# Kernel tuning notes

Hardware: AMD Instinct MI355X
Metric: run time of the kernel (lower is better)

## Reference

```python
import jax, jax.numpy as jnp
import numpy as np

CHANNELS = 32
HIDDEN = 1024
LAYERS = 8
NODE_TYPES = 7
N_NODES = 500_000
N_EDGES = 2_000_000
NUM_GRAPHS = 1024


def setup_inputs() -> dict:
    key = jax.random.key(0)
    ks = jax.random.split(key, 8)
    nodes = jax.random.randint(ks[0], (N_NODES,), 0, NODE_TYPES)
    sources = jax.random.randint(ks[1], (N_EDGES,), 0, N_NODES)
    targets = jax.random.randint(ks[2], (N_EDGES,), 0, N_NODES)
    # sorted graph ids covering all NUM_GRAPHS graphs (no empty graphs)
    batch = (jnp.arange(N_NODES) * NUM_GRAPHS) // N_NODES
    emb = jax.random.normal(ks[3], (NODE_TYPES, CHANNELS), dtype=jnp.float32)
    # xavier-normal-ish init for the 8 layers x {out, back} 32x32 convs
    xavier_std = (2.0 / (CHANNELS + CHANNELS)) ** 0.5
    conv_w = jax.random.normal(ks[4], (LAYERS, 2, CHANNELS, CHANNELS), dtype=jnp.float32) * xavier_std
    hidden_w = jax.random.normal(ks[5], (CHANNELS, HIDDEN), dtype=jnp.float32) * 0.05
    hidden_b = jax.random.normal(ks[6], (HIDDEN,), dtype=jnp.float32) * 0.05
    out_w = jax.random.normal(ks[7], (HIDDEN, 1), dtype=jnp.float32) * 0.05
    return dict(nodes=nodes, sources=sources, targets=targets, batch=batch,
                emb=emb, conv_w=conv_w, hidden_w=hidden_w, hidden_b=hidden_b,
                out_w=out_w)


def reference(nodes, sources, targets, batch, emb, conv_w, hidden_w, hidden_b, out_w):
    n = nodes.shape[0]
    ones_e = jnp.ones(sources.shape[0], dtype=jnp.float32)
    # norm = 1 / (1 + in-degree), norm_t = 1 / (1 + out-degree)  [N,1]
    norm = (1.0 / (1.0 + jax.ops.segment_sum(ones_e, targets, num_segments=n)))[:, None]
    norm_t = (1.0 / (1.0 + jax.ops.segment_sum(ones_e, sources, num_segments=n)))[:, None]
    node_counts = jax.ops.segment_sum(jnp.ones(n, dtype=jnp.float32), batch,
                                      num_segments=NUM_GRAPHS)

    x = emb[nodes]  # [N, C]

    def conv(x, s, t, nrm, w):
        # x.index_add(0, t, x[s]) -> x + scatter_add of gathered source feats
        agg = nrm * (x + jax.ops.segment_sum(x[s], t, num_segments=n))
        return jax.nn.relu(agg @ w)

    for l in range(LAYERS):
        x = x + conv(x, sources, targets, norm, conv_w[l, 0]) \
              + conv(x, targets, sources, norm_t, conv_w[l, 1])

    # mean pooling per graph
    g = jax.ops.segment_sum(x, batch, num_segments=NUM_GRAPHS) / node_counts[:, None]
    h = jax.nn.relu(g @ hidden_w + hidden_b)
    return (h @ out_w).squeeze(-1)  # [NUM_GRAPHS]
```

## Files before the change

### kernel.cpp

```cpp
#include <hip/hip_runtime.h>

#define CHANNELS 32
#define HIDDEN 1024
#define LAYERS 8
#define NRANGE 8

typedef __attribute__((ext_vector_type(8))) short short8;
typedef __attribute__((ext_vector_type(4))) float float4v;

__device__ __forceinline__ short f2bf_rne(float f) {
    union { float f; unsigned u; } v; v.f = f;
    unsigned r = v.u + 0x7fffu + ((v.u >> 16) & 1u);
    return (short)(r >> 16);
}
__device__ __forceinline__ float bfu2f(unsigned short h) {
    union { float f; unsigned u; } v; v.u = ((unsigned)h) << 16;
    return v.f;
}


__global__ __launch_bounds__(256)
void deg_range_kernel(const int* __restrict__ src, const int* __restrict__ tgt,
                      int* __restrict__ deg2, int n_nodes, int n_edges, int rsh) {
    int r = blockIdx.x & (NRANGE - 1);
    int chunk = blockIdx.x >> 3;
    int base = chunk * 2048;
#pragma unroll
    for (int j = 0; j < 8; j++) {
        int e = base + j * 256 + threadIdx.x;
        if (e < n_edges) {
            int t = __builtin_nontemporal_load(tgt + e);
            int s = __builtin_nontemporal_load(src + e);
            if ((t >> rsh) == r) atomicAdd(&deg2[t], 1);
            if ((s >> rsh) == r) atomicAdd(&deg2[n_nodes + s], 1);
        }
    }
}


__global__ __launch_bounds__(256)
void scan_pass1(const int* __restrict__ deg, int* __restrict__ bs, int n) {
    __shared__ int sh[256];
    int t = threadIdx.x;
    int base = blockIdx.x * 2048 + t * 8;
    int s = 0;
#pragma unroll
    for (int j = 0; j < 8; j++) { int idx = base + j; if (idx < n) s += deg[idx]; }
    sh[t] = s; __syncthreads();
    for (int st = 128; st > 0; st >>= 1) { if (t < st) sh[t] += sh[t + st]; __syncthreads(); }
    if (t == 0) bs[blockIdx.x] = sh[0];
}

__global__ void scan_pass2(int* __restrict__ bs, int nb) {
    __shared__ int sh[1024];
    int t = threadIdx.x;
    int v = (t < nb) ? bs[t] : 0;
    sh[t] = v; __syncthreads();
    for (int off = 1; off < 1024; off <<= 1) {
        int u = (t >= off) ? sh[t - off] : 0; __syncthreads();
        sh[t] += u; __syncthreads();
    }
    if (t < nb) bs[t] = sh[t] - v;
}

__global__ __launch_bounds__(256)
void scan_pass3(const int* __restrict__ deg, const int* __restrict__ bs,
                int* __restrict__ off, int n) {
    __shared__ int sh[256];
    int t = threadIdx.x;
    int base = blockIdx.x * 2048 + t * 8;
    int v[8]; int s = 0;
#pragma unroll
    for (int j = 0; j < 8; j++) { int idx = base + j; v[j] = (idx < n) ? deg[idx] : 0; s += v[j]; }
    sh[t] = s; __syncthreads();
    for (int st = 1; st < 256; st <<= 1) {
        int u = (t >= st) ? sh[t - st] : 0; __syncthreads();
        sh[t] += u; __syncthreads();
    }
    int acc = bs[blockIdx.x] + sh[t] - s;
#pragma unroll
    for (int j = 0; j < 8; j++) { int idx = base + j; if (idx < n) off[idx] = acc; acc += v[j]; }
}


__global__ __launch_bounds__(256)
void scatter_range_kernel(const int* __restrict__ src, const int* __restrict__ tgt,
                          int* __restrict__ cur2, int* __restrict__ nbr,
                          int n_nodes, int n_edges, int rsh, int rbase) {
    int r = rbase + (blockIdx.x & (NRANGE - 1));
    int chunk = blockIdx.x >> 3;
    int base = chunk * 2048;
#pragma unroll
    for (int j = 0; j < 8; j++) {
        int e = base + j * 256 + threadIdx.x;
        if (e < n_edges) {
            int t = __builtin_nontemporal_load(tgt + e);
            int s = __builtin_nontemporal_load(src + e);
            if ((t >> rsh) == r) { int p = atomicAdd(&cur2[t], 1);           nbr[p] = s; }
            if ((s >> rsh) == r) { int q = atomicAdd(&cur2[n_nodes + s], 1); nbr[q] = t; }
        }
    }
}


__global__ __launch_bounds__(256)
void init_kernel(const int* __restrict__ nodes, const float* __restrict__ emb,
                 const int* __restrict__ deg2,
                 float* __restrict__ x, unsigned short* __restrict__ xg,
                 float* __restrict__ norm, float* __restrict__ norm_t, int n_nodes) {
    int gid = blockIdx.x * blockDim.x + threadIdx.x;
    int i = gid >> 5, c = gid & 31;
    if (i >= n_nodes) return;
    float v = emb[nodes[i] * CHANNELS + c];
    x[gid] = v;
    xg[gid] = (unsigned short)f2bf_rne(v);
    if (c == 0) {
        norm[i]   = 1.0f / (1.0f + (float)deg2[i]);
        norm_t[i] = 1.0f / (1.0f + (float)deg2[n_nodes + i]);
    }
}


__global__ void counts_kernel(const int* __restrict__ batch, float* __restrict__ counts,
                              int n_nodes, int n_graphs) {
    int b = blockIdx.x * blockDim.x + threadIdx.x;
    if (b >= n_graphs) return;
    int lo = 0, hi = n_nodes;
    while (lo < hi) { int mid = (lo + hi) >> 1; if (batch[mid] < b) lo = mid + 1; else hi = mid; }
    int s = lo;
    lo = 0; hi = n_nodes;
    while (lo < hi) { int mid = (lo + hi) >> 1; if (batch[mid] < b + 1) lo = mid + 1; else hi = mid; }
    counts[b] = (float)(lo - s);
}


__global__ __launch_bounds__(256, 8)
void layer_mfma(const int* __restrict__ off2, const int* __restrict__ nbr,
                const float* __restrict__ wbase,
                const float* __restrict__ norm, const float* __restrict__ norm_t,
                float* __restrict__ x,
                const unsigned short* __restrict__ xgin,
                unsigned short* __restrict__ xgout,
                int n_nodes, int n_edges) {
    __shared__ short A1h[64][32], A2h[64][32];
    __shared__ short W0h[32][32], W1h[32][32];
    __shared__ int offIn[65], offOut[65];

    int tid = threadIdx.x;
    int nodeblock = blockIdx.x * 64;

    for (int idx = tid; idx < CHANNELS * CHANNELS; idx += 256) {
        int k = idx >> 5, n = idx & 31;
        W0h[n][k] = f2bf_rne(wbase[idx]);
        W1h[n][k] = f2bf_rne(wbase[CHANNELS * CHANNELS + idx]);
    }
    if (tid < 65) {
        int idx = nodeblock + tid;
        offIn[tid]  = (idx <= n_nodes) ? off2[idx] : n_edges;
        int idx2 = n_nodes + idx;
        offOut[tid] = (idx2 < 2 * n_nodes) ? off2[idx2] : 2 * n_edges;
    }
    __syncthreads();

    int c = tid & 31, g = tid >> 5;

    int bi_c, d1_c, bo_c, d2_c, nbl1_c, nbl2_c, node_c;
    float xv_c;
    {
        int local = g;
        node_c = nodeblock + local;
        bi_c = offIn[local];  d1_c = offIn[local + 1] - bi_c;
        bo_c = offOut[local]; d2_c = offOut[local + 1] - bo_c;
        nbl1_c = (c < d1_c) ? nbr[bi_c + c] : 0;
        nbl2_c = (c < d2_c) ? nbr[bo_c + c] : 0;
        xv_c = (node_c < n_nodes) ? x[node_c * CHANNELS + c] : 0.f;
    }

    for (int pass = 0; pass < 8; pass++) {
        int bi_n = 0, d1_n = 0, bo_n = 0, d2_n = 0, nbl1_n = 0, nbl2_n = 0, node_n = 0;
        float xv_n = 0.f;
        if (pass < 7) {
            int local = (pass + 1) * 8 + g;
            node_n = nodeblock + local;
            bi_n = offIn[local];  d1_n = offIn[local + 1] - bi_n;
            bo_n = offOut[local]; d2_n = offOut[local + 1] - bo_n;
            nbl1_n = (c < d1_n) ? nbr[bi_n + c] : 0;
            nbl2_n = (c < d2_n) ? nbr[bo_n + c] : 0;
            xv_n = (node_n < n_nodes) ? x[node_n * CHANNELS + c] : 0.f;
        }

        int local = pass * 8 + g;
        int i = node_c;
        int self = (i < n_nodes) ? i : 0;

        int m1 = d1_c < 32 ? d1_c : 32;
        int m2 = d2_c < 32 ? d2_c : 32;
        int mm = m1 > m2 ? m1 : m2;

        float a1 = 0.f, a2 = 0.f;
        for (int j = 0; j < mm; j += 4) {
            int p0 = __shfl(nbl1_c, (j)     & 31, 32);
            int p1 = __shfl(nbl1_c, (j + 1) & 31, 32);
            int p2 = __shfl(nbl1_c, (j + 2) & 31, 32);
            int p3 = __shfl(nbl1_c, (j + 3) & 31, 32);
            int q0 = __shfl(nbl2_c, (j)     & 31, 32);
            int q1 = __shfl(nbl2_c, (j + 1) & 31, 32);
            int q2 = __shfl(nbl2_c, (j + 2) & 31, 32);
            int q3 = __shfl(nbl2_c, (j + 3) & 31, 32);
            p0 = (j     < m1) ? p0 : self;
            p1 = (j + 1 < m1) ? p1 : self;
            p2 = (j + 2 < m1) ? p2 : self;
            p3 = (j + 3 < m1) ? p3 : self;
            q0 = (j     < m2) ? q0 : self;
            q1 = (j + 1 < m2) ? q1 : self;
            q2 = (j + 2 < m2) ? q2 : self;
            q3 = (j + 3 < m2) ? q3 : self;
            float u0 = bfu2f(xgin[p0 * CHANNELS + c]);
            float u1 = bfu2f(xgin[p1 * CHANNELS + c]);
            float u2 = bfu2f(xgin[p2 * CHANNELS + c]);
            float u3 = bfu2f(xgin[p3 * CHANNELS + c]);
            float w0 = bfu2f(xgin[q0 * CHANNELS + c]);
            float w1 = bfu2f(xgin[q1 * CHANNELS + c]);
            float w2 = bfu2f(xgin[q2 * CHANNELS + c]);
            float w3 = bfu2f(xgin[q3 * CHANNELS + c]);
            a1 += (j     < m1) ? u0 : 0.f;
            a1 += (j + 1 < m1) ? u1 : 0.f;
            a1 += (j + 2 < m1) ? u2 : 0.f;
            a1 += (j + 3 < m1) ? u3 : 0.f;
            a2 += (j     < m2) ? w0 : 0.f;
            a2 += (j + 1 < m2) ? w1 : 0.f;
            a2 += (j + 2 < m2) ? w2 : 0.f;
            a2 += (j + 3 < m2) ? w3 : 0.f;
        }
        for (int e = bi_c + 32; e < bi_c + d1_c; e++) a1 += bfu2f(xgin[nbr[e] * CHANNELS + c]);
        for (int e = bo_c + 32; e < bo_c + d2_c; e++) a2 += bfu2f(xgin[nbr[e] * CHANNELS + c]);

        if (i < n_nodes) {
            float n1 = norm[i], n2 = norm_t[i];
            a1 = n1 * (xv_c + a1);
            a2 = n2 * (xv_c + a2);
            A1h[local][c] = f2bf_rne(a1);
            A2h[local][c] = f2bf_rne(a2);
        } else {
            A1h[local][c] = 0;
            A2h[local][c] = 0;
        }

        bi_c = bi_n; d1_c = d1_n; bo_c = bo_n; d2_c = d2_n;
        nbl1_c = nbl1_n; nbl2_c = nbl2_n; xv_c = xv_n; node_c = node_n;
    }
    __syncthreads();

    int wv = tid >> 6, lane = tid & 63;
    int m = lane & 15, quad = lane >> 4;
    int row0 = wv * 16;

    short8 a1h = *(const short8*)&A1h[row0 + m][quad * 8];
    short8 a2h = *(const short8*)&A2h[row0 + m][quad * 8];

    float4v dd[4];
#pragma unroll
    for (int h = 0; h < 2; h++) {
        int n0 = h * 16 + m;
        short8 b0h = *(const short8*)&W0h[n0][quad * 8];
        short8 b1h = *(const short8*)&W1h[n0][quad * 8];
        float4v d1 = {0.f, 0.f, 0.f, 0.f};
        d1 = __builtin_amdgcn_mfma_f32_16x16x32_bf16(a1h, b0h, d1, 0, 0, 0);
        float4v d2 = {0.f, 0.f, 0.f, 0.f};
        d2 = __builtin_amdgcn_mfma_f32_16x16x32_bf16(a2h, b1h, d2, 0, 0, 0);
        dd[h * 2] = d1; dd[h * 2 + 1] = d2;
    }

#pragma unroll
    for (int h = 0; h < 2; h++) {
        float4v d1 = dd[h * 2], d2 = dd[h * 2 + 1];
#pragma unroll
        for (int r = 0; r < 4; r++) {
            int local = row0 + quad * 4 + r;
            int node = nodeblock + local;
            if (node < n_nodes) {
                int col = h * 16 + m;
                float v = x[node * CHANNELS + col] + fmaxf(d1[r], 0.f) + fmaxf(d2[r], 0.f);
                x[node * CHANNELS + col] = v;
                xgout[node * CHANNELS + col] = (unsigned short)f2bf_rne(v);
            }
        }
    }
}


#define POOL_CHUNK 2048

__global__ __launch_bounds__(256)
void pool_kernel(const int* __restrict__ batch, const float* __restrict__ x,
                 float* __restrict__ g, int n_nodes) {
    int c = threadIdx.x & 31;
    int r = threadIdx.x >> 5;
    int base = blockIdx.x * POOL_CHUNK;
    float acc = 0.f;
    int cur = -1;
    for (int it = 0; it < POOL_CHUNK / 8; it++) {
        int node = base + it * 8 + r;
        if (node >= n_nodes) break;
        int b = batch[node];
        if (b != cur) {
            if (cur >= 0) atomicAdd(&g[cur * CHANNELS + c], acc);
            acc = 0.f;
            cur = b;
        }
        acc += x[node * CHANNELS + c];
    }
    if (cur >= 0) atomicAdd(&g[cur * CHANNELS + c], acc);
}


__global__ __launch_bounds__(256)
void mlp_kernel(const float* __restrict__ g, const float* __restrict__ counts,
                const float* __restrict__ hidden_w, const float* __restrict__ hidden_b,
                const float* __restrict__ out_w, float* __restrict__ out) {
    __shared__ float grow[CHANNELS];
    __shared__ float red[256];
    int graph = blockIdx.x;
    int tid = threadIdx.x;
    if (tid < CHANNELS) grow[tid] = g[graph * CHANNELS + tid] / counts[graph];
    __syncthreads();
    float partial = 0.f;
    for (int q = 0; q < HIDDEN / 256; q++) {
        int j = q * 256 + tid;
        float h = hidden_b[j];
#pragma unroll
        for (int k = 0; k < CHANNELS; k++) h += grow[k] * hidden_w[k * HIDDEN + j];
        partial += fmaxf(h, 0.f) * out_w[j];
    }
    red[tid] = partial;
    __syncthreads();
    for (int s = 128; s > 0; s >>= 1) {
        if (tid < s) red[tid] += red[tid + s];
        __syncthreads();
    }
    if (tid == 0) out[graph] = red[0];
}


extern "C" void kernel_launch(void* const* d_in, const int* in_sizes, int n_in,
                              void* d_out, int out_size, void* d_ws, size_t ws_size,
                              hipStream_t stream) {
    const int*   nodes    = (const int*)d_in[0];
    const int*   sources  = (const int*)d_in[1];
    const int*   targets  = (const int*)d_in[2];
    const int*   batch    = (const int*)d_in[3];
    const float* emb      = (const float*)d_in[4];
    const float* conv_w   = (const float*)d_in[5];
    const float* hidden_w = (const float*)d_in[6];
    const float* hidden_b = (const float*)d_in[7];
    const float* out_w    = (const float*)d_in[8];
    float* out = (float*)d_out;

    const int n_nodes  = in_sizes[0];
    const int n_edges  = in_sizes[1];
    const int n_graphs = out_size;
    const int n2 = 2 * n_nodes;

    int rsh8 = 0;
    while (((n_nodes - 1) >> rsh8) >= 8) rsh8++;
    int rsh16 = 0;
    while (((n_nodes - 1) >> rsh16) >= 16) rsh16++;

    char* ws = (char*)d_ws;
    float*          x      = (float*)ws;          ws += (size_t)n_nodes * CHANNELS * 4;
    unsigned short* xg0    = (unsigned short*)ws; ws += (size_t)n_nodes * CHANNELS * 2;
    unsigned short* xg1    = (unsigned short*)ws; ws += (size_t)n_nodes * CHANNELS * 2;
    float* norm   = (float*)ws; ws += (size_t)n_nodes * 4;
    float* norm_t = (float*)ws; ws += (size_t)n_nodes * 4;
    int*   deg2   = (int*)ws;   ws += (size_t)n2 * 4;
    int*   off2   = (int*)ws;   ws += (size_t)n2 * 4;
    int*   cur2   = (int*)ws;   ws += (size_t)n2 * 4;
    int*   nbr    = (int*)ws;   ws += (size_t)2 * n_edges * 4;
    int*   bsums  = (int*)ws;   ws += 4096;
    float* g      = (float*)ws; ws += (size_t)n_graphs * CHANNELS * 4;
    float* counts = (float*)ws; ws += (size_t)n_graphs * 4;

    hipMemsetAsync(deg2, 0, (size_t)n2 * 4, stream);
    hipMemsetAsync(g, 0, (size_t)n_graphs * CHANNELS * 4, stream);

    int echunks = (n_edges + 2047) / 2048;

    deg_range_kernel<<<echunks * NRANGE, 256, 0, stream>>>(sources, targets, deg2,
                                                           n_nodes, n_edges, rsh8);

    int nblk = (n2 + 2047) / 2048;
    scan_pass1<<<nblk, 256, 0, stream>>>(deg2, bsums, n2);
    scan_pass2<<<1, 1024, 0, stream>>>(bsums, nblk);
    scan_pass3<<<nblk, 256, 0, stream>>>(deg2, bsums, off2, n2);

    hipMemcpyAsync(cur2, off2, (size_t)n2 * 4, hipMemcpyDeviceToDevice, stream);
    scatter_range_kernel<<<echunks * NRANGE, 256, 0, stream>>>(sources, targets, cur2, nbr,
                                                               n_nodes, n_edges, rsh16, 0);
    scatter_range_kernel<<<echunks * NRANGE, 256, 0, stream>>>(sources, targets, cur2, nbr,
                                                               n_nodes, n_edges, rsh16, 8);

    int node_thr = n_nodes * CHANNELS;
    init_kernel<<<(node_thr + 255) / 256, 256, 0, stream>>>(nodes, emb, deg2, x, xg0,
                                                            norm, norm_t, n_nodes);
    counts_kernel<<<(n_graphs + 255) / 256, 256, 0, stream>>>(batch, counts, n_nodes, n_graphs);

    unsigned short* xgin = xg0; unsigned short* xgout = xg1;
    int lblocks = (n_nodes + 63) / 64;
    for (int l = 0; l < LAYERS; l++) {
        const float* wbase = conv_w + (size_t)l * 2 * CHANNELS * CHANNELS;
        layer_mfma<<<lblocks, 256, 0, stream>>>(off2, nbr, wbase, norm, norm_t,
                                                x, xgin, xgout, n_nodes, n_edges);
        unsigned short* tmp = xgin; xgin = xgout; xgout = tmp;
    }

    int pool_blocks = (n_nodes + POOL_CHUNK - 1) / POOL_CHUNK;
    pool_kernel<<<pool_blocks, 256, 0, stream>>>(batch, x, g, n_nodes);
    mlp_kernel<<<n_graphs, 256, 0, stream>>>(g, counts, hidden_w, hidden_b, out_w, out);
}
```

Baseline: 1.616 ms.

## Store node state as split bf16 hi/lo pair, derive norms from degrees, fuse prep kernels

The fp32 residual state x is replaced by a bf16 high part, which is ping-ponged and gathered by neighbours, plus a bf16 low-part residual. Self reads and writes therefore move 4 bytes per element instead of 4+2 and the separate fp32 array disappears. The norm arrays are dropped and recomputed from the CSR degree counts already in registers. The degree, embedding-init and count kernels are merged into one launch. The cost is extra conversion arithmetic and slightly lower precision, since hi+lo carries about 16 mantissa bits rather than 24.

```diff
diff --git a/kernel.cpp b/kernel.cpp
--- a/kernel.cpp
+++ b/kernel.cpp
@@ -13,6 +13,10 @@
     unsigned r = v.u + 0x7fffu + ((v.u >> 16) & 1u);
     return (short)(r >> 16);
 }
+__device__ __forceinline__ float bf2f(short h) {
+    union { float f; unsigned u; } v; v.u = ((unsigned)(unsigned short)h) << 16;
+    return v.f;
+}
 __device__ __forceinline__ float bfu2f(unsigned short h) {
     union { float f; unsigned u; } v; v.u = ((unsigned)h) << 16;
     return v.f;
@@ -20,19 +24,47 @@
 
 
 __global__ __launch_bounds__(256)
-void deg_range_kernel(const int* __restrict__ src, const int* __restrict__ tgt,
-                      int* __restrict__ deg2, int n_nodes, int n_edges, int rsh) {
-    int r = blockIdx.x & (NRANGE - 1);
-    int chunk = blockIdx.x >> 3;
-    int base = chunk * 2048;
-#pragma unroll
-    for (int j = 0; j < 8; j++) {
-        int e = base + j * 256 + threadIdx.x;
-        if (e < n_edges) {
-            int t = __builtin_nontemporal_load(tgt + e);
-            int s = __builtin_nontemporal_load(src + e);
-            if ((t >> rsh) == r) atomicAdd(&deg2[t], 1);
-            if ((s >> rsh) == r) atomicAdd(&deg2[n_nodes + s], 1);
+void pre_kernel(const int* __restrict__ src, const int* __restrict__ tgt,
+                int* __restrict__ deg2,
+                const int* __restrict__ nodes, const float* __restrict__ emb,
+                unsigned short* __restrict__ hi0, unsigned short* __restrict__ lo,
+                const int* __restrict__ batch, float* __restrict__ counts,
+                int n_nodes, int n_edges, int n_graphs, int rsh,
+                int degB, int initB) {
+    int bid = blockIdx.x;
+    int tid = threadIdx.x;
+    if (bid < degB) {
+        int r = bid & (NRANGE - 1);
+        int chunk = bid >> 3;
+        int base = chunk * 2048;
+#pragma unroll
+        for (int j = 0; j < 8; j++) {
+            int e = base + j * 256 + tid;
+            if (e < n_edges) {
+                int t = __builtin_nontemporal_load(tgt + e);
+                int s = __builtin_nontemporal_load(src + e);
+                if ((t >> rsh) == r) atomicAdd(&deg2[t], 1);
+                if ((s >> rsh) == r) atomicAdd(&deg2[n_nodes + s], 1);
+            }
+        }
+    } else if (bid < degB + initB) {
+        int gid = (bid - degB) * 256 + tid;
+        int i = gid >> 5, c = gid & 31;
+        if (i < n_nodes) {
+            float v = emb[nodes[i] * CHANNELS + c];
+            short h = f2bf_rne(v);
+            hi0[gid] = (unsigned short)h;
+            lo[gid]  = (unsigned short)f2bf_rne(v - bf2f(h));
+        }
+    } else {
+        int b = (bid - degB - initB) * 256 + tid;
+        if (b < n_graphs) {
+            int lo_i = 0, hi_i = n_nodes;
+            while (lo_i < hi_i) { int mid = (lo_i + hi_i) >> 1; if (batch[mid] < b) lo_i = mid + 1; else hi_i = mid; }
+            int s0 = lo_i;
+            lo_i = 0; hi_i = n_nodes;
+            while (lo_i < hi_i) { int mid = (lo_i + hi_i) >> 1; if (batch[mid] < b + 1) lo_i = mid + 1; else hi_i = mid; }
+            counts[b] = (float)(lo_i - s0);
         }
     }
 }
@@ -103,44 +135,12 @@
 }
 
 
-__global__ __launch_bounds__(256)
-void init_kernel(const int* __restrict__ nodes, const float* __restrict__ emb,
-                 const int* __restrict__ deg2,
-                 float* __restrict__ x, unsigned short* __restrict__ xg,
-                 float* __restrict__ norm, float* __restrict__ norm_t, int n_nodes) {
-    int gid = blockIdx.x * blockDim.x + threadIdx.x;
-    int i = gid >> 5, c = gid & 31;
-    if (i >= n_nodes) return;
-    float v = emb[nodes[i] * CHANNELS + c];
-    x[gid] = v;
-    xg[gid] = (unsigned short)f2bf_rne(v);
-    if (c == 0) {
-        norm[i]   = 1.0f / (1.0f + (float)deg2[i]);
-        norm_t[i] = 1.0f / (1.0f + (float)deg2[n_nodes + i]);
-    }
-}
-
-
-__global__ void counts_kernel(const int* __restrict__ batch, float* __restrict__ counts,
-                              int n_nodes, int n_graphs) {
-    int b = blockIdx.x * blockDim.x + threadIdx.x;
-    if (b >= n_graphs) return;
-    int lo = 0, hi = n_nodes;
-    while (lo < hi) { int mid = (lo + hi) >> 1; if (batch[mid] < b) lo = mid + 1; else hi = mid; }
-    int s = lo;
-    lo = 0; hi = n_nodes;
-    while (lo < hi) { int mid = (lo + hi) >> 1; if (batch[mid] < b + 1) lo = mid + 1; else hi = mid; }
-    counts[b] = (float)(lo - s);
-}
-
-
 __global__ __launch_bounds__(256, 8)
 void layer_mfma(const int* __restrict__ off2, const int* __restrict__ nbr,
                 const float* __restrict__ wbase,
-                const float* __restrict__ norm, const float* __restrict__ norm_t,
-                float* __restrict__ x,
-                const unsigned short* __restrict__ xgin,
-                unsigned short* __restrict__ xgout,
+                const unsigned short* __restrict__ hi_in,
+                unsigned short* __restrict__ hi_out,
+                unsigned short* __restrict__ lo,
                 int n_nodes, int n_edges) {
     __shared__ short A1h[64][32], A2h[64][32];
     __shared__ short W0h[32][32], W1h[32][32];
@@ -173,7 +173,8 @@
         bo_c = offOut[local]; d2_c = offOut[local + 1] - bo_c;
         nbl1_c = (c < d1_c) ? nbr[bi_c + c] : 0;
         nbl2_c = (c < d2_c) ? nbr[bo_c + c] : 0;
-        xv_c = (node_c < n_nodes) ? x[node_c * CHANNELS + c] : 0.f;
+        xv_c = (node_c < n_nodes)
+             ? bfu2f(hi_in[node_c * CHANNELS + c]) + bfu2f(lo[node_c * CHANNELS + c]) : 0.f;
     }
 
     for (int pass = 0; pass < 8; pass++) {
@@ -186,7 +187,8 @@
             bo_n = offOut[local]; d2_n = offOut[local + 1] - bo_n;
             nbl1_n = (c < d1_n) ? nbr[bi_n + c] : 0;
             nbl2_n = (c < d2_n) ? nbr[bo_n + c] : 0;
-            xv_n = (node_n < n_nodes) ? x[node_n * CHANNELS + c] : 0.f;
+            xv_n = (node_n < n_nodes)
+                 ? bfu2f(hi_in[node_n * CHANNELS + c]) + bfu2f(lo[node_n * CHANNELS + c]) : 0.f;
         }
 
         int local = pass * 8 + g;
@@ -215,14 +217,14 @@
             q1 = (j + 1 < m2) ? q1 : self;
             q2 = (j + 2 < m2) ? q2 : self;
             q3 = (j + 3 < m2) ? q3 : self;
-            float u0 = bfu2f(xgin[p0 * CHANNELS + c]);
-            float u1 = bfu2f(xgin[p1 * CHANNELS + c]);
-            float u2 = bfu2f(xgin[p2 * CHANNELS + c]);
-            float u3 = bfu2f(xgin[p3 * CHANNELS + c]);
-            float w0 = bfu2f(xgin[q0 * CHANNELS + c]);
-            float w1 = bfu2f(xgin[q1 * CHANNELS + c]);
-            float w2 = bfu2f(xgin[q2 * CHANNELS + c]);
-            float w3 = bfu2f(xgin[q3 * CHANNELS + c]);
+            float u0 = bfu2f(hi_in[p0 * CHANNELS + c]);
+            float u1 = bfu2f(hi_in[p1 * CHANNELS + c]);
+            float u2 = bfu2f(hi_in[p2 * CHANNELS + c]);
+            float u3 = bfu2f(hi_in[p3 * CHANNELS + c]);
+            float w0 = bfu2f(hi_in[q0 * CHANNELS + c]);
+            float w1 = bfu2f(hi_in[q1 * CHANNELS + c]);
+            float w2 = bfu2f(hi_in[q2 * CHANNELS + c]);
+            float w3 = bfu2f(hi_in[q3 * CHANNELS + c]);
             a1 += (j     < m1) ? u0 : 0.f;
             a1 += (j + 1 < m1) ? u1 : 0.f;
             a1 += (j + 2 < m1) ? u2 : 0.f;
@@ -232,11 +234,12 @@
             a2 += (j + 2 < m2) ? w2 : 0.f;
             a2 += (j + 3 < m2) ? w3 : 0.f;
         }
-        for (int e = bi_c + 32; e < bi_c + d1_c; e++) a1 += bfu2f(xgin[nbr[e] * CHANNELS + c]);
-        for (int e = bo_c + 32; e < bo_c + d2_c; e++) a2 += bfu2f(xgin[nbr[e] * CHANNELS + c]);
+        for (int e = bi_c + 32; e < bi_c + d1_c; e++) a1 += bfu2f(hi_in[nbr[e] * CHANNELS + c]);
+        for (int e = bo_c + 32; e < bo_c + d2_c; e++) a2 += bfu2f(hi_in[nbr[e] * CHANNELS + c]);
 
         if (i < n_nodes) {
-            float n1 = norm[i], n2 = norm_t[i];
+            float n1 = 1.0f / (1.0f + (float)d1_c);
+            float n2 = 1.0f / (1.0f + (float)d2_c);
             a1 = n1 * (xv_c + a1);
             a2 = n2 * (xv_c + a2);
             A1h[local][c] = f2bf_rne(a1);
@@ -280,9 +283,12 @@
             int node = nodeblock + local;
             if (node < n_nodes) {
                 int col = h * 16 + m;
-                float v = x[node * CHANNELS + col] + fmaxf(d1[r], 0.f) + fmaxf(d2[r], 0.f);
-                x[node * CHANNELS + col] = v;
-                xgout[node * CHANNELS + col] = (unsigned short)f2bf_rne(v);
+                size_t idx = (size_t)node * CHANNELS + col;
+                float base = bfu2f(hi_in[idx]) + bfu2f(lo[idx]);
+                float v = base + fmaxf(d1[r], 0.f) + fmaxf(d2[r], 0.f);
+                short hn = f2bf_rne(v);
+                hi_out[idx] = (unsigned short)hn;
+                lo[idx]     = (unsigned short)f2bf_rne(v - bf2f(hn));
             }
         }
     }
@@ -292,7 +298,9 @@
 #define POOL_CHUNK 2048
 
 __global__ __launch_bounds__(256)
-void pool_kernel(const int* __restrict__ batch, const float* __restrict__ x,
+void pool_kernel(const int* __restrict__ batch,
+                 const unsigned short* __restrict__ hi,
+                 const unsigned short* __restrict__ lo,
                  float* __restrict__ g, int n_nodes) {
     int c = threadIdx.x & 31;
     int r = threadIdx.x >> 5;
@@ -308,7 +316,8 @@
             acc = 0.f;
             cur = b;
         }
-        acc += x[node * CHANNELS + c];
+        size_t idx = (size_t)node * CHANNELS + c;
+        acc += bfu2f(hi[idx]) + bfu2f(lo[idx]);
     }
     if (cur >= 0) atomicAdd(&g[cur * CHANNELS + c], acc);
 }
@@ -367,11 +376,9 @@
     while (((n_nodes - 1) >> rsh16) >= 16) rsh16++;
 
     char* ws = (char*)d_ws;
-    float*          x      = (float*)ws;          ws += (size_t)n_nodes * CHANNELS * 4;
-    unsigned short* xg0    = (unsigned short*)ws; ws += (size_t)n_nodes * CHANNELS * 2;
-    unsigned short* xg1    = (unsigned short*)ws; ws += (size_t)n_nodes * CHANNELS * 2;
-    float* norm   = (float*)ws; ws += (size_t)n_nodes * 4;
-    float* norm_t = (float*)ws; ws += (size_t)n_nodes * 4;
+    unsigned short* hi0 = (unsigned short*)ws; ws += (size_t)n_nodes * CHANNELS * 2;
+    unsigned short* hi1 = (unsigned short*)ws; ws += (size_t)n_nodes * CHANNELS * 2;
+    unsigned short* lo  = (unsigned short*)ws; ws += (size_t)n_nodes * CHANNELS * 2;
     int*   deg2   = (int*)ws;   ws += (size_t)n2 * 4;
     int*   off2   = (int*)ws;   ws += (size_t)n2 * 4;
     int*   cur2   = (int*)ws;   ws += (size_t)n2 * 4;
@@ -384,9 +391,15 @@
     hipMemsetAsync(g, 0, (size_t)n_graphs * CHANNELS * 4, stream);
 
     int echunks = (n_edges + 2047) / 2048;
-
-    deg_range_kernel<<<echunks * NRANGE, 256, 0, stream>>>(sources, targets, deg2,
-                                                           n_nodes, n_edges, rsh8);
+    int degB  = echunks * NRANGE;
+    int initB = (n_nodes * CHANNELS + 255) / 256;
+    int cntB  = (n_graphs + 255) / 256;
+
+    pre_kernel<<<degB + initB + cntB, 256, 0, stream>>>(sources, targets, deg2,
+                                                        nodes, emb, hi0, lo,
+                                                        batch, counts,
+                                                        n_nodes, n_edges, n_graphs,
+                                                        rsh8, degB, initB);
 
     int nblk = (n2 + 2047) / 2048;
     scan_pass1<<<nblk, 256, 0, stream>>>(deg2, bsums, n2);
@@ -399,21 +412,16 @@
     scatter_range_kernel<<<echunks * NRANGE, 256, 0, stream>>>(sources, targets, cur2, nbr,
                                                                n_nodes, n_edges, rsh16, 8);
 
-    int node_thr = n_nodes * CHANNELS;
-    init_kernel<<<(node_thr + 255) / 256, 256, 0, stream>>>(nodes, emb, deg2, x, xg0,
-                                                            norm, norm_t, n_nodes);
-    counts_kernel<<<(n_graphs + 255) / 256, 256, 0, stream>>>(batch, counts, n_nodes, n_graphs);
-
-    unsigned short* xgin = xg0; unsigned short* xgout = xg1;
+    unsigned short* hin = hi0; unsigned short* hout = hi1;
     int lblocks = (n_nodes + 63) / 64;
     for (int l = 0; l < LAYERS; l++) {
         const float* wbase = conv_w + (size_t)l * 2 * CHANNELS * CHANNELS;
-        layer_mfma<<<lblocks, 256, 0, stream>>>(off2, nbr, wbase, norm, norm_t,
-                                                x, xgin, xgout, n_nodes, n_edges);
-        unsigned short* tmp = xgin; xgin = xgout; xgout = tmp;
+        layer_mfma<<<lblocks, 256, 0, stream>>>(off2, nbr, wbase,
+                                                hin, hout, lo, n_nodes, n_edges);
+        unsigned short* tmp = hin; hin = hout; hout = tmp;
     }
 
     int pool_blocks = (n_nodes + POOL_CHUNK - 1) / POOL_CHUNK;
-    pool_kernel<<<pool_blocks, 256, 0, stream>>>(batch, x, g, n_nodes);
+    pool_kernel<<<pool_blocks, 256, 0, stream>>>(batch, hin, lo, g, n_nodes);
     mlp_kernel<<<n_graphs, 256, 0, stream>>>(g, counts, hidden_w, hidden_b, out_w, out);
 }
```

New measurement: 1.529 ms. 5.4% less time.
